# Kernel optimization log

Hardware: AMD Instinct MI355X
Metric: run time of the kernel (lower is better)

The kernel has to match this reference:

```python
import jax, jax.numpy as jnp
import numpy as np

N = 100000   # nodes
E = 1600000  # edges (avg degree 16)
F_IN = 128   # num_features
H = 128      # num_hidden
C = 40       # num_classes


def setup_inputs() -> dict:
    key = jax.random.key(0)
    ks = jax.random.split(key, 8)
    w = lambda k, sh: jax.random.normal(k, sh, dtype=jnp.float32) * 0.05
    return {
        "x": jax.random.normal(ks[0], (N, F_IN), dtype=jnp.float32),
        "edge_index": jax.random.randint(ks[1], (2, E), 0, N),
        "W_rel1": w(ks[2], (F_IN, H)),
        "b_rel1": jnp.zeros((H,), jnp.float32),
        "W_root1": w(ks[3], (F_IN, H)),
        "W_rel2": w(ks[4], (H, H)),
        "b_rel2": jnp.zeros((H,), jnp.float32),
        "W_root2": w(ks[5], (H, H)),
        "W_lin": w(ks[6], (2 * H, C)),
        "b_lin": jnp.zeros((C,), jnp.float32),
    }


def _graph_conv(x, src, dst, W_rel, b_rel, W_root, n):
    # PyG GraphConv: sum_{j in N(i)} x_j -> lin_rel, plus lin_root(x_i)
    agg = jax.ops.segment_sum(x[src], dst, num_segments=n)  # [N, d_in]
    return agg @ W_rel + b_rel + x @ W_root


def reference(x, edge_index, W_rel1, b_rel1, W_root1, W_rel2, b_rel2, W_root2, W_lin, b_lin):
    src, dst = edge_index[0], edge_index[1]
    n = x.shape[0]
    # dropout is identity at inference (training=False)
    x1 = jax.nn.relu(_graph_conv(x, src, dst, W_rel1, b_rel1, W_root1, n))
    x2 = jax.nn.relu(_graph_conv(x1, src, dst, W_rel2, b_rel2, W_root2, n))
    h = jnp.concatenate([x1, x2], axis=-1)  # [N, 2H]
    return jax.nn.log_softmax(h @ W_lin + b_lin, axis=-1)
```

## Files before the change

kernel.cpp:

```cpp
#include <hip/hip_runtime.h>
#include <hip/hip_bf16.h>

typedef __attribute__((ext_vector_type(8))) short bf16x8;
typedef __attribute__((ext_vector_type(4))) float f32x4;
typedef __attribute__((ext_vector_type(2))) float f32x2;

#define EPB 4096
#define BUCKET_BITS 8
#define BUCKET_SIZE 256
#define MAXBUCK 512

static __device__ __forceinline__ unsigned short f2bf(float f) {
    union { float f; unsigned u; } v; v.f = f;
    unsigned r = v.u + 0x7FFF + ((v.u >> 16) & 1);
    return (unsigned short)(r >> 16);
}
static __device__ __forceinline__ float asf(unsigned u) {
    union { unsigned u; float f; } v; v.u = u;
    return v.f;
}
static __device__ __forceinline__ f32x2 cvt2(unsigned u) {
    f32x2 r;
    r.x = asf(u << 16);
    r.y = asf(u & 0xFFFF0000u);
    return r;
}

__global__ __launch_bounds__(256) void prep(const float* __restrict__ Wrel1,
                                            const float* __restrict__ Wroot1,
                                            const float* __restrict__ Wrel2,
                                            const float* __restrict__ Wroot2,
                                            const float* __restrict__ Wlin,
                                            const int* __restrict__ dst,
                                            unsigned short* __restrict__ bsw1,
                                            unsigned short* __restrict__ bsw2,
                                            unsigned short* __restrict__ bswL,
                                            int* __restrict__ hist,
                                            int E, int nblk, int nbuck) {
    __shared__ int h[MAXBUCK];
    int blk = blockIdx.x, t = threadIdx.x;
    if (blk < 256) {
        const float* Wrel  = (blk < 128) ? Wrel1 : Wrel2;
        const float* Wroot = (blk < 128) ? Wroot1 : Wroot2;
        unsigned short* bsw = (blk < 128) ? bsw1 : bsw2;
        int idx = (blk & 127) * 256 + t;
        int j = idx & 7, L = (idx >> 3) & 63, ct = (idx >> 9) & 15, kt = idx >> 13;
        int k = kt * 32 + ((L >> 4) * 8) + j;
        int c = ct * 16 + (L & 15);
        float v = (c < 128) ? Wrel[k * 128 + c] : Wroot[k * 128 + (c - 128)];
        bsw[idx] = f2bf(v);
    } else if (blk < 304) {
        int idx = (blk - 256) * 256 + t;
        int tt = idx;
        int j = tt & 7; tt >>= 3;
        int L = tt & 63; tt >>= 6;
        int ct = tt % 3;
        int kt = tt / 3;
        int k = kt * 32 + ((L >> 4) * 8) + j;
        int c = ct * 16 + (L & 15);
        float v = (c < 40) ? Wlin[k * 40 + c] : 0.f;
        bswL[idx] = f2bf(v);
    } else {
        int hb = blk - 304;
        for (int i = t; i < MAXBUCK; i += 256) h[i] = 0;
        __syncthreads();
        int e0 = hb * EPB;
#pragma unroll
        for (int it = 0; it < EPB / 256; it++) {
            int e = e0 + it * 256 + t;
            if (e < E) atomicAdd(&h[dst[e] >> BUCKET_BITS], 1);
        }
        __syncthreads();
        for (int i = t; i < nbuck; i += 256) hist[i * nblk + hb] = h[i];
    }
}

__global__ __launch_bounds__(256) void bucket_total(const int* __restrict__ hist,
                                                    int* __restrict__ total, int nblk) {
    __shared__ int s[256];
    int b = blockIdx.x, t = threadIdx.x;
    int v = 0;
    for (int i = t; i < nblk; i += 256) v += hist[b * nblk + i];
    s[t] = v; __syncthreads();
#pragma unroll
    for (int o = 128; o >= 1; o >>= 1) {
        if (t < o) s[t] += s[t + o];
        __syncthreads();
    }
    if (t == 0) total[b] = s[0];
}

__global__ __launch_bounds__(256) void bucket_scan(const int* __restrict__ total,
                                                   int* __restrict__ base, int nbuck) {
    __shared__ int s[256];
    int t = threadIdx.x;
    int e0 = (2 * t < nbuck) ? total[2 * t] : 0;
    int e1 = (2 * t + 1 < nbuck) ? total[2 * t + 1] : 0;
    int ps = e0 + e1;
    s[t] = ps; __syncthreads();
#pragma unroll
    for (int o = 1; o < 256; o <<= 1) {
        int x = (t >= o) ? s[t - o] : 0;
        __syncthreads();
        s[t] += x; __syncthreads();
    }
    int pbase = s[t] - ps;
    if (2 * t <= nbuck) base[2 * t] = pbase;
    if (2 * t + 1 <= nbuck) base[2 * t + 1] = pbase + e0;
}

__global__ __launch_bounds__(256) void block_scan(int* __restrict__ hist,
                                                  const int* __restrict__ base, int nblk) {
    __shared__ int s[256];
    int b = blockIdx.x, t = threadIdx.x;
    int carryv = base[b];
    for (int start = 0; start < nblk; start += 256) {
        int i = start + t;
        int v = (i < nblk) ? hist[b * nblk + i] : 0;
        s[t] = v; __syncthreads();
#pragma unroll
        for (int o = 1; o < 256; o <<= 1) {
            int x = (t >= o) ? s[t - o] : 0;
            __syncthreads();
            s[t] += x; __syncthreads();
        }
        int excl = s[t] - v + carryv;
        if (i < nblk) hist[b * nblk + i] = excl;
        carryv += s[255];
        __syncthreads();
    }
}

__global__ __launch_bounds__(256) void edge_part(const int* __restrict__ src,
                                                 const int* __restrict__ dst,
                                                 const int* __restrict__ hist,
                                                 int* __restrict__ part,
                                                 int E, int nblk, int nbuck) {
    __shared__ int hcnt[MAXBUCK];
    __shared__ int lstart[MAXBUCK];
    __shared__ int cur[MAXBUCK];
    __shared__ int gbase[MAXBUCK];
    __shared__ int s2[256];
    __shared__ int sdst[EPB];
    __shared__ int ssrc[EPB];
    int t = threadIdx.x, blk = blockIdx.x;
    int e0 = blk * EPB;
    int cnt = E - e0; if (cnt > EPB) cnt = EPB;
    for (int i = t; i < MAXBUCK; i += 256) hcnt[i] = 0;
    for (int i = t; i < nbuck; i += 256) gbase[i] = hist[i * nblk + blk];
    __syncthreads();
    int myd[EPB / 256], mys[EPB / 256];
#pragma unroll
    for (int it = 0; it < EPB / 256; it++) {
        int i = it * 256 + t;
        if (i < cnt) {
            myd[it] = dst[e0 + i];
            mys[it] = src[e0 + i];
            atomicAdd(&hcnt[myd[it] >> BUCKET_BITS], 1);
        }
    }
    __syncthreads();
    int p0 = hcnt[2 * t], p1 = hcnt[2 * t + 1];
    int ps = p0 + p1;
    s2[t] = ps; __syncthreads();
#pragma unroll
    for (int o = 1; o < 256; o <<= 1) {
        int x = (t >= o) ? s2[t - o] : 0;
        __syncthreads();
        s2[t] += x; __syncthreads();
    }
    int pbase = s2[t] - ps;
    lstart[2 * t] = pbase; lstart[2 * t + 1] = pbase + p0;
    cur[2 * t] = 0; cur[2 * t + 1] = 0;
    __syncthreads();
#pragma unroll
    for (int it = 0; it < EPB / 256; it++) {
        int i = it * 256 + t;
        if (i < cnt) {
            int b = myd[it] >> BUCKET_BITS;
            int p = lstart[b] + atomicAdd(&cur[b], 1);
            sdst[p] = myd[it];
            ssrc[p] = mys[it];
        }
    }
    __syncthreads();
    for (int i = t; i < cnt; i += 256) {
        int d = sdst[i], s = ssrc[i];
        int b = d >> BUCKET_BITS;
        part[gbase[b] + (i - lstart[b])] = ((d & (BUCKET_SIZE - 1)) << 17) | s;
    }
}

__global__ __launch_bounds__(256) void csrfin_gemm1(const int* __restrict__ part,
                                                    const int* __restrict__ bucketBase,
                                                    int* __restrict__ off_,
                                                    int* __restrict__ deg_,
                                                    int* __restrict__ csr_src,
                                                    const float* __restrict__ x,
                                                    const unsigned short* __restrict__ Bsw,
                                                    const float* __restrict__ bias,
                                                    unsigned short* __restrict__ xr,
                                                    unsigned short* __restrict__ accbf,
                                                    int N, int nbuck) {
    __shared__ int cur[BUCKET_SIZE];
    __shared__ int h[BUCKET_SIZE];
    __shared__ int tsum[256];
    int t = threadIdx.x;
    if (blockIdx.x < (unsigned)nbuck) {
        int b = blockIdx.x;
        int lo = bucketBase[b], hi = bucketBase[b + 1];
        int n0 = b * BUCKET_SIZE;
        h[t] = 0;
        __syncthreads();
        for (int i = lo + t; i < hi; i += 256) atomicAdd(&h[part[i] >> 17], 1);
        __syncthreads();
        int hv = h[t];
        tsum[t] = hv;
        __syncthreads();
#pragma unroll
        for (int o = 1; o < 256; o <<= 1) {
            int xx = (t >= o) ? tsum[t - o] : 0;
            __syncthreads();
            tsum[t] += xx;
            __syncthreads();
        }
        int st = tsum[t] - hv;
        cur[t] = st;
        int node = n0 + t;
        if (node < N) { off_[node] = lo + st; deg_[node] = hv; }
        __syncthreads();
        for (int i = lo + t; i < hi; i += 256) {
            int rec = part[i];
            int p = atomicAdd(&cur[rec >> 17], 1);
            csr_src[lo + p] = rec & 0x1FFFF;
        }
    } else {
        int wid = (blockIdx.x - nbuck) * 4 + (t >> 6);
        int L = t & 63;
        int r0 = wid * 16;
        if (r0 >= N) return;
        int arow = r0 + (L & 15);
        const bf16x8* Bptr = ((const bf16x8*)Bsw) + L;
        f32x4 acc[16];
#pragma unroll
        for (int i = 0; i < 16; i++) acc[i] = (f32x4){0.f, 0.f, 0.f, 0.f};
#pragma unroll
        for (int kt = 0; kt < 4; kt++) {
            const float* Arow = x + (size_t)arow * 128 + ((L >> 4) * 8) + kt * 32;
            float4 a0 = *(const float4*)Arow;
            float4 a1 = *(const float4*)(Arow + 4);
            bf16x8 a;
            a[0] = (short)f2bf(a0.x); a[1] = (short)f2bf(a0.y);
            a[2] = (short)f2bf(a0.z); a[3] = (short)f2bf(a0.w);
            a[4] = (short)f2bf(a1.x); a[5] = (short)f2bf(a1.y);
            a[6] = (short)f2bf(a1.z); a[7] = (short)f2bf(a1.w);
#pragma unroll
            for (int ct = 0; ct < 16; ct++) {
                bf16x8 b = Bptr[(kt * 16 + ct) * 64];
                acc[ct] = __builtin_amdgcn_mfma_f32_16x16x32_bf16(a, b, acc[ct], 0, 0, 0);
            }
        }
        int rbase = r0 + (L >> 4) * 4;
        int cl = L & 15;
#pragma unroll
        for (int ct = 0; ct < 16; ct++) {
            int col = ct * 16 + cl;
#pragma unroll
            for (int r = 0; r < 4; r++) {
                int row = rbase + r;
                float v = acc[ct][r];
                if (col < 128)
                    xr[(size_t)row * 128 + col] = f2bf(v);
                else
                    accbf[(size_t)row * 128 + (col - 128)] = f2bf(v + bias[col - 128]);
            }
        }
    }
}

__global__ __launch_bounds__(256) void gemm_layer2(const unsigned short* __restrict__ Abf,
                                                   const unsigned short* __restrict__ Bsw,
                                                   const float* __restrict__ bias,
                                                   unsigned short* __restrict__ xr,
                                                   unsigned short* __restrict__ accbf, int N) {
    __shared__ unsigned short Bs[32768];
    int t = threadIdx.x;
    {
        uint4* d4 = (uint4*)Bs;
        const uint4* s4 = (const uint4*)Bsw;
#pragma unroll
        for (int i = 0; i < 16; i++) d4[t + i * 256] = s4[t + i * 256];
    }
    __syncthreads();
    int w = t >> 6, L = t & 63;
    int nTiles = (N + 15) / 16;
    for (int tile = blockIdx.x * 4 + w; tile < nTiles; tile += gridDim.x * 4) {
        int r0 = tile * 16;
        int arow = r0 + (L & 15);
        f32x4 acc[16];
#pragma unroll
        for (int i = 0; i < 16; i++) acc[i] = (f32x4){0.f, 0.f, 0.f, 0.f};
#pragma unroll
        for (int kt = 0; kt < 4; kt++) {
            bf16x8 a = *((const bf16x8*)(Abf + (size_t)arow * 128 + ((L >> 4) * 8) + kt * 32));
#pragma unroll
            for (int ct = 0; ct < 16; ct++) {
                bf16x8 b = *(const bf16x8*)(Bs + (((kt * 16 + ct) * 64) + L) * 8);
                acc[ct] = __builtin_amdgcn_mfma_f32_16x16x32_bf16(a, b, acc[ct], 0, 0, 0);
            }
        }
        int rbase = r0 + (L >> 4) * 4;
        int cl = L & 15;
#pragma unroll
        for (int ct = 0; ct < 16; ct++) {
            int col = ct * 16 + cl;
#pragma unroll
            for (int r = 0; r < 4; r++) {
                int row = rbase + r;
                float v = acc[ct][r];
                if (col < 128)
                    xr[(size_t)row * 128 + col] = f2bf(v);
                else
                    accbf[(size_t)row * 128 + (col - 128)] = f2bf(v + bias[col - 128]);
            }
        }
    }
}

__global__ __launch_bounds__(256) void agg_relu_cvt(const unsigned short* __restrict__ xr,
                                                    const unsigned short* __restrict__ accbf,
                                                    const int* __restrict__ off_,
                                                    const int* __restrict__ deg,
                                                    const int* __restrict__ csr_src,
                                                    unsigned short* __restrict__ out, int N) {
    int node = blockIdx.x * 4 + (threadIdx.x >> 6);
    if (node >= N) return;
    int L = threadIdx.x & 63;
    int g = L >> 4;
    int f = L & 15;
    int o = off_[node];
    int d = deg[node];
    uint4 arow = (uint4){0, 0, 0, 0};
    if (g == 0) arow = *(const uint4*)(accbf + (size_t)node * 128 + f * 8);

    const int* ip = csr_src + o + g;
    const unsigned short* xrf = xr + f * 8;

    f32x2 a0 = (f32x2){0.f, 0.f}, a1 = (f32x2){0.f, 0.f};
    f32x2 a2 = (f32x2){0.f, 0.f}, a3 = (f32x2){0.f, 0.f};

    int d4 = d & ~3;
#pragma unroll 4
    for (int k = 0; k < d4; k += 4) {
        int s = ip[k];
        uint4 p = *(const uint4*)(xrf + (size_t)s * 128);
        a0 += cvt2(p.x);
        a1 += cvt2(p.y);
        a2 += cvt2(p.z);
        a3 += cvt2(p.w);
    }
    if (d4 + g < d) {
        int s = ip[d4];
        uint4 p = *(const uint4*)(xrf + (size_t)s * 128);
        a0 += cvt2(p.x);
        a1 += cvt2(p.y);
        a2 += cvt2(p.z);
        a3 += cvt2(p.w);
    }
    a0.x += __shfl_xor(a0.x, 16, 64); a0.y += __shfl_xor(a0.y, 16, 64);
    a1.x += __shfl_xor(a1.x, 16, 64); a1.y += __shfl_xor(a1.y, 16, 64);
    a2.x += __shfl_xor(a2.x, 16, 64); a2.y += __shfl_xor(a2.y, 16, 64);
    a3.x += __shfl_xor(a3.x, 16, 64); a3.y += __shfl_xor(a3.y, 16, 64);
    a0.x += __shfl_xor(a0.x, 32, 64); a0.y += __shfl_xor(a0.y, 32, 64);
    a1.x += __shfl_xor(a1.x, 32, 64); a1.y += __shfl_xor(a1.y, 32, 64);
    a2.x += __shfl_xor(a2.x, 32, 64); a2.y += __shfl_xor(a2.y, 32, 64);
    a3.x += __shfl_xor(a3.x, 32, 64); a3.y += __shfl_xor(a3.y, 32, 64);

    if (g == 0) {
        uint4 wv;
        wv.x = ((unsigned)f2bf(fmaxf(asf(arow.x & 0xFFFF0000u) + a0.y, 0.f)) << 16)
             | f2bf(fmaxf(asf(arow.x << 16) + a0.x, 0.f));
        wv.y = ((unsigned)f2bf(fmaxf(asf(arow.y & 0xFFFF0000u) + a1.y, 0.f)) << 16)
             | f2bf(fmaxf(asf(arow.y << 16) + a1.x, 0.f));
        wv.z = ((unsigned)f2bf(fmaxf(asf(arow.z & 0xFFFF0000u) + a2.y, 0.f)) << 16)
             | f2bf(fmaxf(asf(arow.z << 16) + a2.x, 0.f));
        wv.w = ((unsigned)f2bf(fmaxf(asf(arow.w & 0xFFFF0000u) + a3.y, 0.f)) << 16)
             | f2bf(fmaxf(asf(arow.w << 16) + a3.x, 0.f));
        *(uint4*)(out + (size_t)node * 128 + f * 8) = wv;
    }
}

__global__ __launch_bounds__(256) void gemm_final_ls(const unsigned short* __restrict__ x1bf,
                                                     const unsigned short* __restrict__ x2bf,
                                                     const unsigned short* __restrict__ Bsw,
                                                     const float* __restrict__ blin,
                                                     float* __restrict__ out, int N) {
    __shared__ unsigned short Bs[12288];
    int t = threadIdx.x;
    {
        uint4* d4 = (uint4*)Bs;
        const uint4* s4 = (const uint4*)Bsw;
#pragma unroll
        for (int i = 0; i < 6; i++) d4[t + i * 256] = s4[t + i * 256];
    }
    __syncthreads();
    int w = t >> 6, L = t & 63;
    int cl = L & 15;
    float b0 = blin[cl], b1 = blin[16 + cl];
    float b2 = (cl < 8) ? blin[32 + cl] : 0.f;
    int nTiles = (N + 15) / 16;
    for (int tile = blockIdx.x * 4 + w; tile < nTiles; tile += gridDim.x * 4) {
        int r0 = tile * 16;
        int arow = r0 + (L & 15);
        f32x4 acc[3];
#pragma unroll
        for (int i = 0; i < 3; i++) acc[i] = (f32x4){0.f, 0.f, 0.f, 0.f};
#pragma unroll
        for (int kt = 0; kt < 8; kt++) {
            const unsigned short* Ab = (kt < 4) ? x1bf : x2bf;
            int kk = (kt & 3) * 32 + ((L >> 4) * 8);
            bf16x8 a = *((const bf16x8*)(Ab + (size_t)arow * 128 + kk));
#pragma unroll
            for (int ct = 0; ct < 3; ct++) {
                bf16x8 b = *(const bf16x8*)(Bs + (((kt * 3 + ct) * 64) + L) * 8);
                acc[ct] = __builtin_amdgcn_mfma_f32_16x16x32_bf16(a, b, acc[ct], 0, 0, 0);
            }
        }
        int rbase = r0 + (L >> 4) * 4;
#pragma unroll
        for (int r = 0; r < 4; r++) {
            int row = rbase + r;
            float v0 = acc[0][r] + b0;
            float v1 = acc[1][r] + b1;
            float v2 = (cl < 8) ? (acc[2][r] + b2) : -__builtin_inff();
            float m = fmaxf(fmaxf(v0, v1), v2);
#pragma unroll
            for (int off = 8; off >= 1; off >>= 1) m = fmaxf(m, __shfl_xor(m, off, 64));
            float e = __expf(v0 - m) + __expf(v1 - m) + ((cl < 8) ? __expf(v2 - m) : 0.f);
#pragma unroll
            for (int off = 8; off >= 1; off >>= 1) e += __shfl_xor(e, off, 64);
            float ls = m + __logf(e);
            float* op = out + (size_t)row * 40;
            op[cl] = v0 - ls;
            op[16 + cl] = v1 - ls;
            if (cl < 8) op[32 + cl] = v2 - ls;
        }
    }
}

extern "C" void kernel_launch(void* const* d_in, const int* in_sizes, int n_in,
                              void* d_out, int out_size, void* d_ws, size_t ws_size,
                              hipStream_t stream) {
    const float* x      = (const float*)d_in[0];
    const int*   edge   = (const int*)d_in[1];
    const float* Wrel1  = (const float*)d_in[2];
    const float* brel1  = (const float*)d_in[3];
    const float* Wroot1 = (const float*)d_in[4];
    const float* Wrel2  = (const float*)d_in[5];
    const float* brel2  = (const float*)d_in[6];
    const float* Wroot2 = (const float*)d_in[7];
    const float* Wlin   = (const float*)d_in[8];
    const float* blin   = (const float*)d_in[9];

    const int N = in_sizes[0] / 128;
    const int E = in_sizes[1] / 2;
    const int* src = edge;
    const int* dst = edge + E;

    const int nblk  = (E + EPB - 1) / EPB;
    const int nbuck = (N + BUCKET_SIZE - 1) / BUCKET_SIZE;

    char* ws = (char*)d_ws;
    size_t off = 0;
    auto alloc = [&](size_t bytes) -> void* {
        void* p = ws + off;
        off += (bytes + 255) & ~(size_t)255;
        return p;
    };
    unsigned short* x1bf = (unsigned short*)alloc((size_t)N * 128 * 2);
    unsigned short* x2bf = (unsigned short*)alloc((size_t)N * 128 * 2);
    unsigned short* xr   = (unsigned short*)alloc((size_t)N * 128 * 2);
    unsigned short* accbf= (unsigned short*)alloc((size_t)N * 128 * 2);
    unsigned short* bsw1 = (unsigned short*)alloc(32768 * 2);
    unsigned short* bsw2 = (unsigned short*)alloc(32768 * 2);
    unsigned short* bswL = (unsigned short*)alloc(12288 * 2);
    int* hist       = (int*)alloc((size_t)nbuck * nblk * 4);
    int* bucketTot  = (int*)alloc((size_t)nbuck * 4);
    int* bucketBase = (int*)alloc((size_t)(nbuck + 1) * 4);
    int* part       = (int*)alloc((size_t)E * 4);
    int* csr_src    = (int*)alloc((size_t)E * 4);
    int* off_       = (int*)alloc((size_t)N * 4);
    int* deg_       = (int*)alloc((size_t)N * 4);

    const int rowTiles = (N + 15) / 16;
    const int gemmBlocks = (rowTiles + 3) / 4;
    const int nodeBlocks = (N + 3) / 4;

    prep<<<304 + nblk, 256, 0, stream>>>(Wrel1, Wroot1, Wrel2, Wroot2, Wlin, dst,
                                         bsw1, bsw2, bswL, hist, E, nblk, nbuck);
    bucket_total<<<nbuck, 256, 0, stream>>>(hist, bucketTot, nblk);
    bucket_scan<<<1, 256, 0, stream>>>(bucketTot, bucketBase, nbuck);
    block_scan<<<nbuck, 256, 0, stream>>>(hist, bucketBase, nblk);
    edge_part<<<nblk, 256, 0, stream>>>(src, dst, hist, part, E, nblk, nbuck);
    csrfin_gemm1<<<nbuck + gemmBlocks, 256, 0, stream>>>(part, bucketBase, off_, deg_, csr_src,
                                                         x, bsw1, brel1, xr, accbf, N, nbuck);
    agg_relu_cvt<<<nodeBlocks, 256, 0, stream>>>(xr, accbf, off_, deg_, csr_src, x1bf, N);
    gemm_layer2<<<512, 256, 0, stream>>>(x1bf, bsw2, brel2, xr, accbf, N);
    agg_relu_cvt<<<nodeBlocks, 256, 0, stream>>>(xr, accbf, off_, deg_, csr_src, x2bf, N);
    gemm_final_ls<<<512, 256, 0, stream>>>(x1bf, x2bf, bswL, blin, (float*)d_out, N);
}
```

Before: 340.0 us.

## Store node features in 16-column slices and aggregate one slice per block

Feature matrices (xr, accbf, x1bf, x2bf) move from row-major [N,128] to 8 column slices of [N,16]. The GEMMs now write and read that layout, and a new aggregation kernel gives each block one slice for 32 nodes, with 8 lanes per node each handling 2 features. The goal is to keep each slice's gather working set (about 3.2MB) resident in cache across the blocks that share it. Each gather is now a 4-byte load, more blocks read the CSR index list, and the per-node loop is serial with only one-step index prefetch, which may expose memory latency.

After: 564.5 us. 1.66x slower.

```diff
diff --git a/kernel.cpp b/kernel.cpp
--- a/kernel.cpp
+++ b/kernel.cpp
@@ -264,15 +264,15 @@
         int cl = L & 15;
 #pragma unroll
         for (int ct = 0; ct < 16; ct++) {
-            int col = ct * 16 + cl;
 #pragma unroll
             for (int r = 0; r < 4; r++) {
                 int row = rbase + r;
                 float v = acc[ct][r];
-                if (col < 128)
-                    xr[(size_t)row * 128 + col] = f2bf(v);
+                if (ct < 8)
+                    xr[((size_t)ct * N + row) * 16 + cl] = f2bf(v);
                 else
-                    accbf[(size_t)row * 128 + (col - 128)] = f2bf(v + bias[col - 128]);
+                    accbf[((size_t)(ct - 8) * N + row) * 16 + cl] =
+                        f2bf(v + bias[(ct - 8) * 16 + cl]);
             }
         }
     }
@@ -302,7 +302,8 @@
         for (int i = 0; i < 16; i++) acc[i] = (f32x4){0.f, 0.f, 0.f, 0.f};
 #pragma unroll
         for (int kt = 0; kt < 4; kt++) {
-            bf16x8 a = *((const bf16x8*)(Abf + (size_t)arow * 128 + ((L >> 4) * 8) + kt * 32));
+            int k0 = (L >> 4) * 8 + kt * 32;
+            bf16x8 a = *((const bf16x8*)(Abf + ((size_t)(k0 >> 4) * N + arow) * 16 + (k0 & 15)));
 #pragma unroll
             for (int ct = 0; ct < 16; ct++) {
                 bf16x8 b = *(const bf16x8*)(Bs + (((kt * 16 + ct) * 64) + L) * 8);
@@ -313,81 +314,54 @@
         int cl = L & 15;
 #pragma unroll
         for (int ct = 0; ct < 16; ct++) {
-            int col = ct * 16 + cl;
 #pragma unroll
             for (int r = 0; r < 4; r++) {
                 int row = rbase + r;
                 float v = acc[ct][r];
-                if (col < 128)
-                    xr[(size_t)row * 128 + col] = f2bf(v);
+                if (ct < 8)
+                    xr[((size_t)ct * N + row) * 16 + cl] = f2bf(v);
                 else
-                    accbf[(size_t)row * 128 + (col - 128)] = f2bf(v + bias[col - 128]);
+                    accbf[((size_t)(ct - 8) * N + row) * 16 + cl] =
+                        f2bf(v + bias[(ct - 8) * 16 + cl]);
             }
         }
     }
 }
 
-__global__ __launch_bounds__(256) void agg_relu_cvt(const unsigned short* __restrict__ xr,
-                                                    const unsigned short* __restrict__ accbf,
-                                                    const int* __restrict__ off_,
-                                                    const int* __restrict__ deg,
-                                                    const int* __restrict__ csr_src,
-                                                    unsigned short* __restrict__ out, int N) {
-    int node = blockIdx.x * 4 + (threadIdx.x >> 6);
+__global__ __launch_bounds__(256) void agg_sliced(const unsigned short* __restrict__ xr,
+                                                  const unsigned short* __restrict__ accbf,
+                                                  const int* __restrict__ off_,
+                                                  const int* __restrict__ deg,
+                                                  const int* __restrict__ csr_src,
+                                                  unsigned short* __restrict__ out, int N) {
+    int s = blockIdx.x & 7;
+    int nb = blockIdx.x >> 3;
+    int t = threadIdx.x;
+    int node = nb * 32 + (t >> 3);
     if (node >= N) return;
-    int L = threadIdx.x & 63;
-    int g = L >> 4;
-    int f = L & 15;
-    int o = off_[node];
-    int d = deg[node];
-    uint4 arow = (uint4){0, 0, 0, 0};
-    if (g == 0) arow = *(const uint4*)(accbf + (size_t)node * 128 + f * 8);
-
-    const int* ip = csr_src + o + g;
-    const unsigned short* xrf = xr + f * 8;
-
-    f32x2 a0 = (f32x2){0.f, 0.f}, a1 = (f32x2){0.f, 0.f};
-    f32x2 a2 = (f32x2){0.f, 0.f}, a3 = (f32x2){0.f, 0.f};
-
-    int d4 = d & ~3;
-#pragma unroll 4
-    for (int k = 0; k < d4; k += 4) {
-        int s = ip[k];
-        uint4 p = *(const uint4*)(xrf + (size_t)s * 128);
-        a0 += cvt2(p.x);
-        a1 += cvt2(p.y);
-        a2 += cvt2(p.z);
-        a3 += cvt2(p.w);
-    }
-    if (d4 + g < d) {
-        int s = ip[d4];
-        uint4 p = *(const uint4*)(xrf + (size_t)s * 128);
-        a0 += cvt2(p.x);
-        a1 += cvt2(p.y);
-        a2 += cvt2(p.z);
-        a3 += cvt2(p.w);
-    }
-    a0.x += __shfl_xor(a0.x, 16, 64); a0.y += __shfl_xor(a0.y, 16, 64);
-    a1.x += __shfl_xor(a1.x, 16, 64); a1.y += __shfl_xor(a1.y, 16, 64);
-    a2.x += __shfl_xor(a2.x, 16, 64); a2.y += __shfl_xor(a2.y, 16, 64);
-    a3.x += __shfl_xor(a3.x, 16, 64); a3.y += __shfl_xor(a3.y, 16, 64);
-    a0.x += __shfl_xor(a0.x, 32, 64); a0.y += __shfl_xor(a0.y, 32, 64);
-    a1.x += __shfl_xor(a1.x, 32, 64); a1.y += __shfl_xor(a1.y, 32, 64);
-    a2.x += __shfl_xor(a2.x, 32, 64); a2.y += __shfl_xor(a2.y, 32, 64);
-    a3.x += __shfl_xor(a3.x, 32, 64); a3.y += __shfl_xor(a3.y, 32, 64);
-
-    if (g == 0) {
-        uint4 wv;
-        wv.x = ((unsigned)f2bf(fmaxf(asf(arow.x & 0xFFFF0000u) + a0.y, 0.f)) << 16)
-             | f2bf(fmaxf(asf(arow.x << 16) + a0.x, 0.f));
-        wv.y = ((unsigned)f2bf(fmaxf(asf(arow.y & 0xFFFF0000u) + a1.y, 0.f)) << 16)
-             | f2bf(fmaxf(asf(arow.y << 16) + a1.x, 0.f));
-        wv.z = ((unsigned)f2bf(fmaxf(asf(arow.z & 0xFFFF0000u) + a2.y, 0.f)) << 16)
-             | f2bf(fmaxf(asf(arow.z << 16) + a2.x, 0.f));
-        wv.w = ((unsigned)f2bf(fmaxf(asf(arow.w & 0xFFFF0000u) + a3.y, 0.f)) << 16)
-             | f2bf(fmaxf(asf(arow.w << 16) + a3.x, 0.f));
-        *(uint4*)(out + (size_t)node * 128 + f * 8) = wv;
-    }
+    int f = t & 7;
+    int o = __builtin_nontemporal_load(off_ + node);
+    int d = __builtin_nontemporal_load(deg + node);
+    const unsigned short* xrs = xr + (size_t)s * N * 16 + f * 2;
+    const int* ip = csr_src + o;
+    f32x2 acc = (f32x2){0.f, 0.f};
+    if (d > 0) {
+        int idx = __builtin_nontemporal_load(ip);
+        for (int k = 1; k < d; k++) {
+            int nidx = __builtin_nontemporal_load(ip + k);
+            unsigned u = *(const unsigned*)(xrs + (size_t)idx * 16);
+            acc += cvt2(u);
+            idx = nidx;
+        }
+        unsigned u = *(const unsigned*)(xrs + (size_t)idx * 16);
+        acc += cvt2(u);
+    }
+    size_t nodeOff = ((size_t)s * N + node) * 16 + f * 2;
+    unsigned ab = __builtin_nontemporal_load((const unsigned*)(accbf + nodeOff));
+    f32x2 av = cvt2(ab);
+    unsigned wv = ((unsigned)f2bf(fmaxf(av.y + acc.y, 0.f)) << 16)
+                | f2bf(fmaxf(av.x + acc.x, 0.f));
+    __builtin_nontemporal_store(wv, (unsigned*)(out + nodeOff));
 }
 
 __global__ __launch_bounds__(256) void gemm_final_ls(const unsigned short* __restrict__ x1bf,
@@ -419,7 +393,7 @@
         for (int kt = 0; kt < 8; kt++) {
             const unsigned short* Ab = (kt < 4) ? x1bf : x2bf;
             int kk = (kt & 3) * 32 + ((L >> 4) * 8);
-            bf16x8 a = *((const bf16x8*)(Ab + (size_t)arow * 128 + kk));
+            bf16x8 a = *((const bf16x8*)(Ab + ((size_t)(kk >> 4) * N + arow) * 16 + (kk & 15)));
 #pragma unroll
             for (int ct = 0; ct < 3; ct++) {
                 bf16x8 b = *(const bf16x8*)(Bs + (((kt * 3 + ct) * 64) + L) * 8);
@@ -494,7 +468,7 @@
 
     const int rowTiles = (N + 15) / 16;
     const int gemmBlocks = (rowTiles + 3) / 4;
-    const int nodeBlocks = (N + 3) / 4;
+    const int aggBlocks = ((N + 31) / 32) * 8;
 
     prep<<<304 + nblk, 256, 0, stream>>>(Wrel1, Wroot1, Wrel2, Wroot2, Wlin, dst,
                                          bsw1, bsw2, bswL, hist, E, nblk, nbuck);
@@ -504,8 +478,8 @@
     edge_part<<<nblk, 256, 0, stream>>>(src, dst, hist, part, E, nblk, nbuck);
     csrfin_gemm1<<<nbuck + gemmBlocks, 256, 0, stream>>>(part, bucketBase, off_, deg_, csr_src,
                                                          x, bsw1, brel1, xr, accbf, N, nbuck);
-    agg_relu_cvt<<<nodeBlocks, 256, 0, stream>>>(xr, accbf, off_, deg_, csr_src, x1bf, N);
+    agg_sliced<<<aggBlocks, 256, 0, stream>>>(xr, accbf, off_, deg_, csr_src, x1bf, N);
     gemm_layer2<<<512, 256, 0, stream>>>(x1bf, bsw2, brel2, xr, accbf, N);
-    agg_relu_cvt<<<nodeBlocks, 256, 0, stream>>>(xr, accbf, off_, deg_, csr_src, x2bf, N);
+    agg_sliced<<<aggBlocks, 256, 0, stream>>>(xr, accbf, off_, deg_, csr_src, x2bf, N);
     gemm_final_ls<<<512, 256, 0, stream>>>(x1bf, x2bf, bswL, blin, (float*)d_out, N);
 }
```
